# Kernel optimization log

Measured on AMD Instinct MI355X. Metric: run time of the kernel, lower is better.

The kernel has to match this reference:

```python
import jax, jax.numpy as jnp
import numpy as np

D_MODEL = 1024
HEADS = 16
HEAD_DIM = D_MODEL // HEADS


def setup_inputs() -> dict:
    key = jax.random.key(0)
    k_x, k_q, k_k, k_v, k_o = jax.random.split(key, 5)
    x = jax.random.normal(k_x, (4, 2048, D_MODEL), dtype=jnp.float32)
    W_q = jax.random.normal(k_q, (D_MODEL, D_MODEL), dtype=jnp.float32)
    W_k = jax.random.normal(k_k, (D_MODEL, D_MODEL), dtype=jnp.float32)
    W_v = jax.random.normal(k_v, (D_MODEL, D_MODEL), dtype=jnp.float32)
    fc_out = jax.random.normal(k_o, (D_MODEL, D_MODEL), dtype=jnp.float32)
    return {"x": x, "W_q": W_q, "W_k": W_k, "W_v": W_v, "fc_out": fc_out}


def reference(x, W_q, W_k, W_v, fc_out):
    b, s, d = x.shape
    h, hd = HEADS, HEAD_DIM
    # Projections: [b, s, d]
    Q = x @ W_q
    K = x @ W_k
    V = x @ W_v
    # Split heads: [b, h, s, hd]
    Q = Q.reshape(b, s, h, hd).transpose(0, 2, 1, 3)
    K = K.reshape(b, s, h, hd).transpose(0, 2, 1, 3)
    V = V.reshape(b, s, h, hd).transpose(0, 2, 1, 3)
    # Scaled dot-product attention (softmax over key axis, per row)
    scores = jnp.einsum('bhqd,bhkd->bhqk', Q, K) / jnp.sqrt(jnp.float32(hd))
    attn = jax.nn.softmax(scores, axis=-1)
    head_out = jnp.einsum('bhqk,bhkd->bhqd', attn, V)
    # Concat heads back: [b, s, d]
    concat = head_out.transpose(0, 2, 1, 3).reshape(b, s, d)
    return concat @ fc_out
```

## Files before the change

### kernel.cpp

```cpp
#include <hip/hip_runtime.h>
#include <hip/hip_fp16.h>

#define BATCH   4
#define SEQ     2048
#define DM      1024
#define HEADS   16
#define HD      64
#define M_TOK   (BATCH * SEQ)
#define QK_LD   2048

#define QSCALE  0.1803368801111204f

typedef __attribute__((ext_vector_type(8)))  _Float16 half8;
typedef __attribute__((ext_vector_type(4)))  float    f32x4;
typedef __attribute__((ext_vector_type(16))) float    f32x16;

__device__ __forceinline__ unsigned short f2h(float x) {
    return __half_as_ushort(__float2half(x));
}
__device__ __forceinline__ float h2f(unsigned short u) {
    return __half2float(__ushort_as_half(u));
}
__device__ __forceinline__ float fast_exp2(float x) {
    float r; asm volatile("v_exp_f32 %0, %1" : "=v"(r) : "v"(x)); return r;
}
__device__ __forceinline__ unsigned int pk2(float a, float b) {
    __fp16 __attribute__((ext_vector_type(2))) h =
        __builtin_amdgcn_cvt_pkrtz(a, b);
    return __builtin_bit_cast(unsigned int, h);
}
__device__ __forceinline__ void dma16(const void* g, void* l) {
    __builtin_amdgcn_global_load_lds(
        (const __attribute__((address_space(1))) void*)g,
        (__attribute__((address_space(3))) void*)l, 16, 0, 0);
}

__global__ __launch_bounds__(256) void split_cast(
    const float* __restrict__ x, unsigned short* __restrict__ hi,
    unsigned short* __restrict__ lo)
{
    const int i = (blockIdx.x * 256 + threadIdx.x) * 8;
    float4 a = *(const float4*)(x + i);
    float4 b = *(const float4*)(x + i + 4);
    float v[8] = {a.x, a.y, a.z, a.w, b.x, b.y, b.z, b.w};
    unsigned short hb[8], lb[8];
#pragma unroll
    for (int j = 0; j < 8; ++j) {
        hb[j] = f2h(v[j]);
        lb[j] = f2h(v[j] - h2f(hb[j]));
    }
    *(float4*)(hi + i) = *(float4*)hb;
    *(float4*)(lo + i) = *(float4*)lb;
}

template<int SPLIT>
__global__ __launch_bounds__(256) void wtrans(
    const float* __restrict__ W, unsigned short* __restrict__ Th_out,
    unsigned short* __restrict__ Tl_out, float scale)
{
    __shared__ unsigned short Th[64][72];
    __shared__ unsigned short Tl[SPLIT ? 64 : 1][72];
    const int t  = threadIdx.x;
    const int n0 = blockIdx.x * 64, k0 = blockIdx.y * 64;
    const int kr = t >> 2, cg = (t & 3) << 4;
#pragma unroll
    for (int jj = 0; jj < 16; jj += 4) {
        float4 wv = *(const float4*)(W + (size_t)(k0 + kr) * DM + n0 + cg + jj);
        float vv[4] = {wv.x, wv.y, wv.z, wv.w};
#pragma unroll
        for (int j = 0; j < 4; ++j) {
            float v = vv[j] * scale;
            unsigned short h = f2h(v);
            Th[cg + jj + j][kr] = h;
            if (SPLIT) Tl[cg + jj + j][kr] = f2h(v - h2f(h));
        }
    }
    __syncthreads();
    const int nr = t >> 2, kg = (t & 3) << 4;
    size_t go = (size_t)(n0 + nr) * DM + k0 + kg;
    *(float4*)(Th_out + go)     = *(float4*)&Th[nr][kg];
    *(float4*)(Th_out + go + 8) = *(float4*)&Th[nr][kg + 8];
    if (SPLIT) {
        *(float4*)(Tl_out + go)     = *(float4*)&Tl[nr][kg];
        *(float4*)(Tl_out + go + 8) = *(float4*)&Tl[nr][kg + 8];
    }
}

template<int PASSES, int EPI>
__global__ __launch_bounds__(256, 2) void gemm_f16(
    const unsigned short* __restrict__ Ah, const unsigned short* __restrict__ Al,
    const unsigned short* __restrict__ Bh, const unsigned short* __restrict__ Bl,
    void* __restrict__ O0, void* __restrict__ O1, int M, int N, int K)
{
    __shared__ unsigned short As_h[2][128 * 32];
    __shared__ unsigned short Bs_h[2][128 * 32];
    __shared__ unsigned short As_l[PASSES == 3 ? 2 : 1][PASSES == 3 ? 128 * 32 : 16];
    __shared__ unsigned short Bs_l[PASSES == 3 ? 2 : 1][PASSES == 3 ? 128 * 32 : 16];

    const int t = threadIdx.x;
    const int w = t >> 6, lane = t & 63, quad = lane >> 4, l15 = lane & 15;
    const int wm = w >> 1, wn = w & 1;
    const int m0 = blockIdx.y * 128, n0 = blockIdx.x * 128;

    const int drow = w * 32 + (lane >> 2);
    const int dcol = (lane & 3) * 8;

    auto stage = [&](int buf, int k0) {
#pragma unroll
        for (int inst = 0; inst < 2; ++inst) {
            const size_t ga = (size_t)(m0 + drow + inst * 16) * K + k0 + dcol;
            const size_t gb = (size_t)(n0 + drow + inst * 16) * K + k0 + dcol;
            const int lo = (w * 32 + inst * 16) * 32;
            dma16(Ah + ga, &As_h[buf][lo]);
            dma16(Bh + gb, &Bs_h[buf][lo]);
            if (PASSES == 3) {
                dma16(Al + ga, &As_l[buf][lo]);
                dma16(Bl + gb, &Bs_l[buf][lo]);
            }
        }
    };

    f32x4 acc[4][4];
#pragma unroll
    for (int mt = 0; mt < 4; ++mt)
#pragma unroll
        for (int nt = 0; nt < 4; ++nt)
#pragma unroll
            for (int r = 0; r < 4; ++r) acc[mt][nt][r] = 0.f;

    const int NIT = K >> 5;
    stage(0, 0);
    for (int it = 0; it < NIT; ++it) {
        __syncthreads();
        const int cur = it & 1;
        if (it + 1 < NIT) stage(cur ^ 1, (it + 1) * 32);

        half8 aH[4], bH[4], aL[4], bL[4];
#pragma unroll
        for (int mt = 0; mt < 4; ++mt) {
            const int row = wm * 64 + mt * 16 + l15;
            aH[mt] = *(const half8*)&As_h[cur][row * 32 + quad * 8];
            if (PASSES == 3) aL[mt] = *(const half8*)&As_l[cur][row * 32 + quad * 8];
        }
#pragma unroll
        for (int nt = 0; nt < 4; ++nt) {
            const int row = wn * 64 + nt * 16 + l15;
            bH[nt] = *(const half8*)&Bs_h[cur][row * 32 + quad * 8];
            if (PASSES == 3) bL[nt] = *(const half8*)&Bs_l[cur][row * 32 + quad * 8];
        }
#pragma unroll
        for (int mt = 0; mt < 4; ++mt)
#pragma unroll
            for (int nt = 0; nt < 4; ++nt) {
                acc[mt][nt] = __builtin_amdgcn_mfma_f32_16x16x32_f16(
                    aH[mt], bH[nt], acc[mt][nt], 0, 0, 0);
                if (PASSES == 3) {
                    acc[mt][nt] = __builtin_amdgcn_mfma_f32_16x16x32_f16(
                        aH[mt], bL[nt], acc[mt][nt], 0, 0, 0);
                    acc[mt][nt] = __builtin_amdgcn_mfma_f32_16x16x32_f16(
                        aL[mt], bH[nt], acc[mt][nt], 0, 0, 0);
                }
            }
    }

#pragma unroll
    for (int mt = 0; mt < 4; ++mt)
#pragma unroll
        for (int nt = 0; nt < 4; ++nt) {
            const int row0 = m0 + wm * 64 + mt * 16 + quad * 4;
            const int col  = n0 + wn * 64 + nt * 16 + l15;
            if (EPI == 0) {
#pragma unroll
                for (int r = 0; r < 4; ++r)
                    ((float*)O0)[(size_t)(row0 + r) * N + col] = acc[mt][nt][r];
            } else if (EPI == 1) {
#pragma unroll
                for (int r = 0; r < 4; ++r) {
                    float v = acc[mt][nt][r];
                    unsigned short h = f2h(v);
                    ((unsigned short*)O0)[(size_t)(row0 + r) * N + col] = h;
                    ((unsigned short*)O1)[(size_t)(row0 + r) * N + col] =
                        f2h(v - h2f(h));
                }
            } else if (EPI == 2) {
#pragma unroll
                for (int r = 0; r < 4; ++r)
                    ((unsigned short*)O0)[(size_t)(row0 + r) * N + col] =
                        f2h(acc[mt][nt][r]);
            } else {
                const int b = row0 >> 11, s = row0 & 2047;
                const int hh = col >> 6, d = col & 63;
                unsigned short vs[4];
#pragma unroll
                for (int r = 0; r < 4; ++r) vs[r] = f2h(acc[mt][nt][r]);
                *(ushort4*)((unsigned short*)O0 +
                            (((size_t)(b * HEADS + hh)) * HD + d) * SEQ + s) =
                    *(ushort4*)vs;
            }
        }
}

__global__ __launch_bounds__(256, 2) void attn_f16(
    const unsigned short* __restrict__ QKh,
    const unsigned short* __restrict__ QKl,
    const unsigned short* __restrict__ Vt,
    unsigned short* __restrict__ Oc)
{
    __shared__ unsigned short SM[2][3 * 4096];

    const int t = threadIdx.x;
    const int w = t >> 6, lane = t & 63;
    const int g = lane >> 5, l31 = lane & 31;
    const int b = blockIdx.z, h = blockIdx.y, q0 = blockIdx.x * 256;

    const size_t row0   = (size_t)b * SEQ;
    const size_t qcol   = (size_t)h * HD;
    const size_t kcol   = 1024 + qcol;
    const size_t vtbase = ((size_t)(b * HEADS + h)) * HD * SEQ;

    const int rl  = lane >> 3;
    const int sw8 = ((lane & 7) ^ (rl & 7)) * 8;
    const int x7  = l31 & 7;

    auto stage = [&](int buf, int k0) {
#pragma unroll
        for (int inst = 0; inst < 2; ++inst) {
            const int r8 = w * 16 + inst * 8;
            const size_t gk = (row0 + k0 + r8 + rl) * QK_LD + kcol + sw8;
            const int lo = r8 * 64;
            dma16(QKh + gk, &SM[buf][lo]);
            dma16(QKl + gk, &SM[buf][4096 + lo]);
            const size_t gv = vtbase + (size_t)(r8 + rl) * SEQ + k0 + sw8;
            dma16(Vt + gv, &SM[buf][8192 + lo]);
        }
    };

    half8 bQh[2][4], bQl[2][4];
#pragma unroll
    for (int qs = 0; qs < 2; ++qs) {
        const size_t qr = (row0 + q0 + qs * 128 + w * 32 + l31) * QK_LD + qcol;
#pragma unroll
        for (int ks = 0; ks < 4; ++ks) {
            bQh[qs][ks] = *(const half8*)(QKh + qr + ks * 16 + g * 8);
            bQl[qs][ks] = *(const half8*)(QKl + qr + ks * 16 + g * 8);
        }
    }

    f32x16 o_acc[2][2];
#pragma unroll
    for (int qs = 0; qs < 2; ++qs)
#pragma unroll
        for (int mt = 0; mt < 2; ++mt)
#pragma unroll
            for (int r = 0; r < 16; ++r) o_acc[qs][mt][r] = 0.f;
    float m_r[2] = {-3.0e38f, -3.0e38f}, l_r[2] = {0.f, 0.f};

    stage(0, 0);
    const int NIT = SEQ / 64;
    for (int it = 0; it < NIT; ++it) {
        __syncthreads();
        const int cur = it & 1;
        if (it + 1 < NIT) stage(cur ^ 1, (it + 1) * 64);
        const unsigned short* Ks  = &SM[cur][0];
        const unsigned short* Ksl = &SM[cur][4096];
        const unsigned short* Vs  = &SM[cur][8192];

        f32x16 s[2][2];
#pragma unroll
        for (int qs = 0; qs < 2; ++qs)
#pragma unroll
            for (int kt = 0; kt < 2; ++kt)
#pragma unroll
                for (int r = 0; r < 16; ++r) s[qs][kt][r] = 0.f;
#pragma unroll
        for (int kt = 0; kt < 2; ++kt)
#pragma unroll
            for (int ks = 0; ks < 4; ++ks) {
                const int off = (kt * 32 + l31) * 64 + (((ks * 2 + g) ^ x7) * 8);
                half8 aKh = *(const half8*)&Ks[off];
                half8 aKl = *(const half8*)&Ksl[off];
#pragma unroll
                for (int qs = 0; qs < 2; ++qs) {
                    s[qs][kt] = __builtin_amdgcn_mfma_f32_32x32x16_f16(
                        aKh, bQh[qs][ks], s[qs][kt], 0, 0, 0);
                    s[qs][kt] = __builtin_amdgcn_mfma_f32_32x32x16_f16(
                        aKl, bQh[qs][ks], s[qs][kt], 0, 0, 0);
                    s[qs][kt] = __builtin_amdgcn_mfma_f32_32x32x16_f16(
                        aKh, bQl[qs][ks], s[qs][kt], 0, 0, 0);
                }
            }

        half8 bP[2][4];
#pragma unroll
        for (int qs = 0; qs < 2; ++qs) {
            float mx = s[qs][0][0];
#pragma unroll
            for (int kt = 0; kt < 2; ++kt)
#pragma unroll
                for (int r = 0; r < 16; ++r) mx = fmaxf(mx, s[qs][kt][r]);
            mx = fmaxf(mx, __shfl_xor(mx, 32));
            const float nm = fmaxf(m_r[qs], mx);
            const float al = fast_exp2(m_r[qs] - nm);
            m_r[qs] = nm;
            float rs = 0.f;
#pragma unroll
            for (int kt = 0; kt < 2; ++kt)
#pragma unroll
                for (int r = 0; r < 16; ++r) {
                    float pv = fast_exp2(s[qs][kt][r] - nm);
                    s[qs][kt][r] = pv;
                    rs += pv;
                }
            rs += __shfl_xor(rs, 32);
            l_r[qs] = l_r[qs] * al + rs;
#pragma unroll
            for (int mt = 0; mt < 2; ++mt)
#pragma unroll
                for (int r = 0; r < 16; ++r) o_acc[qs][mt][r] *= al;

#pragma unroll
            for (int kt = 0; kt < 2; ++kt)
#pragma unroll
                for (int ksl = 0; ksl < 2; ++ksl) {
                    const int base = ksl * 8;
                    unsigned int lo0 = pk2(s[qs][kt][base + 0], s[qs][kt][base + 1]);
                    unsigned int lo1 = pk2(s[qs][kt][base + 2], s[qs][kt][base + 3]);
                    unsigned int hi0 = pk2(s[qs][kt][base + 4], s[qs][kt][base + 5]);
                    unsigned int hi1 = pk2(s[qs][kt][base + 6], s[qs][kt][base + 7]);
                    unsigned int s0 = g ? lo0 : hi0;
                    unsigned int s1 = g ? lo1 : hi1;
                    unsigned int r0 = (unsigned int)__shfl_xor((int)s0, 32);
                    unsigned int r1 = (unsigned int)__shfl_xor((int)s1, 32);
                    union { unsigned int u[4]; half8 hv; } u;
                    u.u[0] = g ? r0 : lo0;
                    u.u[1] = g ? r1 : lo1;
                    u.u[2] = g ? hi0 : r0;
                    u.u[3] = g ? hi1 : r1;
                    bP[qs][kt * 2 + ksl] = u.hv;
                }
        }

#pragma unroll
        for (int mt = 0; mt < 2; ++mt)
#pragma unroll
            for (int kk = 0; kk < 4; ++kk) {
                const int off = (mt * 32 + l31) * 64 + (((kk * 2 + g) ^ x7) * 8);
                half8 aV = *(const half8*)&Vs[off];
#pragma unroll
                for (int qs = 0; qs < 2; ++qs)
                    o_acc[qs][mt] = __builtin_amdgcn_mfma_f32_32x32x16_f16(
                        aV, bP[qs][kk], o_acc[qs][mt], 0, 0, 0);
            }
    }

#pragma unroll
    for (int qs = 0; qs < 2; ++qs) {
        const float inv = 1.0f / l_r[qs];
        unsigned short* orow =
            Oc + (row0 + q0 + qs * 128 + w * 32 + l31) * DM + h * HD;
#pragma unroll
        for (int mt = 0; mt < 2; ++mt)
#pragma unroll
            for (int rq = 0; rq < 4; ++rq) {
                unsigned int w0 = pk2(o_acc[qs][mt][rq * 4 + 0] * inv,
                                      o_acc[qs][mt][rq * 4 + 1] * inv);
                unsigned int w1 = pk2(o_acc[qs][mt][rq * 4 + 2] * inv,
                                      o_acc[qs][mt][rq * 4 + 3] * inv);
                const int d0 = mt * 32 + rq * 8 + g * 4;
                uint2 pkd; pkd.x = w0; pkd.y = w1;
                *(uint2*)(orow + d0) = pkd;
            }
    }
}

extern "C" void kernel_launch(void* const* d_in, const int* in_sizes, int n_in,
                              void* d_out, int out_size, void* d_ws, size_t ws_size,
                              hipStream_t stream) {
    const float* x  = (const float*)d_in[0];
    const float* Wq = (const float*)d_in[1];
    const float* Wk = (const float*)d_in[2];
    const float* Wv = (const float*)d_in[3];
    const float* Wo = (const float*)d_in[4];
    float* out = (float*)d_out;

    char* ws = (char*)d_ws;
    const size_t SZ_TOK = (size_t)M_TOK * DM * 2;
    const size_t SZ_W   = (size_t)DM * DM * 2;

    unsigned short* xh     = (unsigned short*)(ws);
    unsigned short* xl     = (unsigned short*)(ws + SZ_TOK);
    unsigned short* Wqkt_h = (unsigned short*)(ws + 2 * SZ_TOK);
    unsigned short* Wqkt_l = (unsigned short*)(ws + 2 * SZ_TOK + 2 * SZ_W);
    unsigned short* Wvt    = (unsigned short*)(ws + 2 * SZ_TOK + 4 * SZ_W);
    unsigned short* Wot    = (unsigned short*)(ws + 2 * SZ_TOK + 5 * SZ_W);
    unsigned short* QKh    = (unsigned short*)(ws + 2 * SZ_TOK + 6 * SZ_W);
    unsigned short* QKl    = (unsigned short*)(ws + 4 * SZ_TOK + 6 * SZ_W);
    unsigned short* Vt_    = (unsigned short*)(ws + 6 * SZ_TOK + 6 * SZ_W);
    unsigned short* concat = xh;

    dim3 blk(256);

    hipLaunchKernelGGL(split_cast, dim3(M_TOK * DM / (256 * 8)), blk, 0, stream,
                       x, xh, xl);
    dim3 wgrid(DM / 64, DM / 64);
    hipLaunchKernelGGL((wtrans<1>), wgrid, blk, 0, stream, Wq, Wqkt_h, Wqkt_l,
                       QSCALE);
    hipLaunchKernelGGL((wtrans<1>), wgrid, blk, 0, stream, Wk,
                       Wqkt_h + (size_t)DM * DM, Wqkt_l + (size_t)DM * DM, 1.0f);
    hipLaunchKernelGGL((wtrans<0>), wgrid, blk, 0, stream, Wv, Wvt, nullptr, 1.0f);
    hipLaunchKernelGGL((wtrans<0>), wgrid, blk, 0, stream, Wo, Wot, nullptr, 1.0f);

    dim3 gqk(QK_LD / 128, M_TOK / 128);
    hipLaunchKernelGGL((gemm_f16<3, 1>), gqk, blk, 0, stream,
                       xh, xl, Wqkt_h, Wqkt_l, QKh, QKl, M_TOK, QK_LD, DM);
    dim3 ggrid(DM / 128, M_TOK / 128);
    hipLaunchKernelGGL((gemm_f16<1, 3>), ggrid, blk, 0, stream,
                       xh, nullptr, Wvt, nullptr, Vt_, nullptr, M_TOK, DM, DM);

    dim3 agrid(SEQ / 256, HEADS, BATCH);
    hipLaunchKernelGGL(attn_f16, agrid, blk, 0, stream, QKh, QKl, Vt_, concat);

    hipLaunchKernelGGL((gemm_f16<1, 0>), ggrid, blk, 0, stream,
                       concat, nullptr, Wot, nullptr, out, nullptr, M_TOK, DM, DM);
}
```

Before: 412.7 us.

## Restructure attention softmax loop with lazy rescale, setprio, and interleaved PV MFMA

Reworks the flash-attention inner loop. The max and sum reductions now use trees so they do not form serial chains. Rescaling of the output accumulator is skipped unless the running max grows by more than 8 (log2 units), and the accumulator is not zero-initialised separately. s_setprio is raised around the MFMA sections, and the PV MFMAs are issued per query subtile so they can overlap with the next subtile's softmax. Removing volatile from v_exp lets the compiler schedule the exp instructions. The lazy rescale allows exponents up to 2^8 before renormalising, which the fp16 P conversion must tolerate.

```diff
diff --git a/kernel.cpp b/kernel.cpp
--- a/kernel.cpp
+++ b/kernel.cpp
@@ -22,7 +22,7 @@
     return __half2float(__ushort_as_half(u));
 }
 __device__ __forceinline__ float fast_exp2(float x) {
-    float r; asm volatile("v_exp_f32 %0, %1" : "=v"(r) : "v"(x)); return r;
+    float r; asm("v_exp_f32 %0, %1" : "=v"(r) : "v"(x)); return r;
 }
 __device__ __forceinline__ unsigned int pk2(float a, float b) {
     __fp16 __attribute__((ext_vector_type(2))) h =
@@ -255,6 +255,10 @@
             for (int r = 0; r < 16; ++r) o_acc[qs][mt][r] = 0.f;
     float m_r[2] = {-3.0e38f, -3.0e38f}, l_r[2] = {0.f, 0.f};
 
+    f32x16 z16;
+#pragma unroll
+    for (int r = 0; r < 16; ++r) z16[r] = 0.f;
+
     stage(0, 0);
     const int NIT = SEQ / 64;
     for (int it = 0; it < NIT; ++it) {
@@ -266,12 +270,7 @@
         const unsigned short* Vs  = &SM[cur][8192];
 
         f32x16 s[2][2];
-#pragma unroll
-        for (int qs = 0; qs < 2; ++qs)
-#pragma unroll
-            for (int kt = 0; kt < 2; ++kt)
-#pragma unroll
-                for (int r = 0; r < 16; ++r) s[qs][kt][r] = 0.f;
+        __builtin_amdgcn_s_setprio(1);
 #pragma unroll
         for (int kt = 0; kt < 2; ++kt)
 #pragma unroll
@@ -282,42 +281,55 @@
 #pragma unroll
                 for (int qs = 0; qs < 2; ++qs) {
                     s[qs][kt] = __builtin_amdgcn_mfma_f32_32x32x16_f16(
-                        aKh, bQh[qs][ks], s[qs][kt], 0, 0, 0);
+                        aKh, bQh[qs][ks], ks == 0 ? z16 : s[qs][kt], 0, 0, 0);
                     s[qs][kt] = __builtin_amdgcn_mfma_f32_32x32x16_f16(
                         aKl, bQh[qs][ks], s[qs][kt], 0, 0, 0);
                     s[qs][kt] = __builtin_amdgcn_mfma_f32_32x32x16_f16(
                         aKh, bQl[qs][ks], s[qs][kt], 0, 0, 0);
                 }
             }
-
-        half8 bP[2][4];
+        __builtin_amdgcn_s_setprio(0);
+
 #pragma unroll
         for (int qs = 0; qs < 2; ++qs) {
-            float mx = s[qs][0][0];
-#pragma unroll
-            for (int kt = 0; kt < 2; ++kt)
-#pragma unroll
-                for (int r = 0; r < 16; ++r) mx = fmaxf(mx, s[qs][kt][r]);
+            float t16[16];
+#pragma unroll
+            for (int r = 0; r < 16; ++r)
+                t16[r] = fmaxf(s[qs][0][r], s[qs][1][r]);
+#pragma unroll
+            for (int st = 8; st > 0; st >>= 1)
+#pragma unroll
+                for (int r = 0; r < st; ++r)
+                    t16[r] = fmaxf(t16[r], t16[r + st]);
+            float mx = t16[0];
             mx = fmaxf(mx, __shfl_xor(mx, 32));
-            const float nm = fmaxf(m_r[qs], mx);
-            const float al = fast_exp2(m_r[qs] - nm);
-            m_r[qs] = nm;
-            float rs = 0.f;
+
+            float nm = m_r[qs];
+            if (!__all(mx <= nm + 8.f)) {
+                nm = fmaxf(nm, mx);
+                const float al = fast_exp2(m_r[qs] - nm);
+                m_r[qs] = nm;
+                l_r[qs] *= al;
+#pragma unroll
+                for (int mt = 0; mt < 2; ++mt)
+#pragma unroll
+                    for (int r = 0; r < 16; ++r) o_acc[qs][mt][r] *= al;
+            }
+
+            float rsv[4] = {0.f, 0.f, 0.f, 0.f};
 #pragma unroll
             for (int kt = 0; kt < 2; ++kt)
 #pragma unroll
                 for (int r = 0; r < 16; ++r) {
                     float pv = fast_exp2(s[qs][kt][r] - nm);
                     s[qs][kt][r] = pv;
-                    rs += pv;
-                }
+                    rsv[r & 3] += pv;
+                }
+            float rs = (rsv[0] + rsv[1]) + (rsv[2] + rsv[3]);
             rs += __shfl_xor(rs, 32);
-            l_r[qs] = l_r[qs] * al + rs;
-#pragma unroll
-            for (int mt = 0; mt < 2; ++mt)
-#pragma unroll
-                for (int r = 0; r < 16; ++r) o_acc[qs][mt][r] *= al;
-
+            l_r[qs] += rs;
+
+            half8 bP[4];
 #pragma unroll
             for (int kt = 0; kt < 2; ++kt)
 #pragma unroll
@@ -336,21 +348,21 @@
                     u.u[1] = g ? r1 : lo1;
                     u.u[2] = g ? hi0 : r0;
                     u.u[3] = g ? hi1 : r1;
-                    bP[qs][kt * 2 + ksl] = u.hv;
-                }
-        }
-
-#pragma unroll
-        for (int mt = 0; mt < 2; ++mt)
-#pragma unroll
-            for (int kk = 0; kk < 4; ++kk) {
-                const int off = (mt * 32 + l31) * 64 + (((kk * 2 + g) ^ x7) * 8);
-                half8 aV = *(const half8*)&Vs[off];
-#pragma unroll
-                for (int qs = 0; qs < 2; ++qs)
+                    bP[kt * 2 + ksl] = u.hv;
+                }
+
+            __builtin_amdgcn_s_setprio(1);
+#pragma unroll
+            for (int mt = 0; mt < 2; ++mt)
+#pragma unroll
+                for (int kk = 0; kk < 4; ++kk) {
+                    const int off = (mt * 32 + l31) * 64 + (((kk * 2 + g) ^ x7) * 8);
+                    half8 aV = *(const half8*)&Vs[off];
                     o_acc[qs][mt] = __builtin_amdgcn_mfma_f32_32x32x16_f16(
-                        aV, bP[qs][kk], o_acc[qs][mt], 0, 0, 0);
-            }
+                        aV, bP[kk], o_acc[qs][mt], 0, 0, 0);
+                }
+            __builtin_amdgcn_s_setprio(0);
+        }
     }
 
 #pragma unroll
```

Measured after the change: 443.3 us. 1.07x slower.
